# Kernel tuning notes

Measured on AMD Instinct MI355X. Metric: run time of the kernel, lower is better.

## Reference

```python
import jax, jax.numpy as jnp
import numpy as np

N, E = 50000, 800000
IN_CH, H, OUT_CH, ED, L = 64, 128, 128, 1, 4


def setup_inputs() -> dict:
    key = jax.random.key(0)
    ks = jax.random.split(key, 24)
    s = 0.02
    inp = {
        'h': jax.random.normal(ks[0], (N, IN_CH), jnp.float32),
        'coords': jax.random.normal(ks[1], (N, 3), jnp.float32),
        'edge_attr': jax.random.normal(ks[2], (E, ED), jnp.float32),
        'emb_in_W': jax.random.normal(ks[3], (IN_CH, H), jnp.float32) * s,
        'emb_in_b': jnp.zeros((H,), jnp.float32),
        'emb_out_W': jax.random.normal(ks[4], (H, OUT_CH), jnp.float32) * s,
        'emb_out_b': jnp.zeros((OUT_CH,), jnp.float32),
        # per-layer stacked params
        'eW1': jax.random.normal(ks[5], (L, 2 * H + 1 + ED, H), jnp.float32) * s,
        'eb1': jnp.zeros((L, H), jnp.float32),
        'eW2': jax.random.normal(ks[6], (L, H, H), jnp.float32) * s,
        'eb2': jnp.zeros((L, H), jnp.float32),
        'cW1': jax.random.normal(ks[7], (L, H, H), jnp.float32) * s,
        'cb1': jnp.zeros((L, H), jnp.float32),
        'cWc': jax.random.normal(ks[8], (L, H, 1), jnp.float32) * 0.001,  # xavier gain=0.001, no bias
        'nW1': jax.random.normal(ks[9], (L, 2 * H, H), jnp.float32) * s,
        'nb1': jnp.zeros((L, H), jnp.float32),
        'nW2': jax.random.normal(ks[10], (L, H, H), jnp.float32) * s,
        'nb2': jnp.zeros((L, H), jnp.float32),
        'edge_index': jax.random.randint(ks[11], (2, E), 0, N, jnp.int32),
    }
    return inp


def _egnn_forward(h, coords, edge_attr, emb_in_W, emb_in_b, emb_out_W, emb_out_b,
                  eW1, eb1, eW2, eb2, cW1, cb1, cWc, nW1, nb1, nW2, nb2, edge_index):
    silu = jax.nn.silu
    row, col = edge_index[0], edge_index[1]  # PyG: j=source=row, i=target=col
    # count of incoming edges per target node, for coords_agg='mean'
    counts = jax.ops.segment_sum(jnp.ones((E,), jnp.float32), col, num_segments=N)
    counts = jnp.maximum(counts, 1.0)[:, None]
    h = h @ emb_in_W + emb_in_b
    for l in range(L):
        coord_diff = coords[row] - coords[col]                       # [E,3]
        dist = jnp.sum(coord_diff * coord_diff, axis=-1, keepdims=True)  # [E,1]
        # message: edge MLP on cat(x_i, x_j, dist, edge_attr)
        edge_in = jnp.concatenate([h[col], h[row], dist, edge_attr], axis=-1)
        ef = silu(edge_in @ eW1[l] + eb1[l])
        ef = silu(ef @ eW2[l] + eb2[l])                               # [E,H]
        cw = silu(ef @ cW1[l] + cb1[l]) @ cWc[l]                      # [E,1]
        coord_upd = coord_diff * cw                                   # [E,3]
        # aggregate to target nodes
        agg_feat = jax.ops.segment_sum(ef, col, num_segments=N)       # [N,H]
        agg_coord = jax.ops.segment_sum(coord_upd, col, num_segments=N) / counts
        # node update (residual)
        node_in = jnp.concatenate([h, agg_feat], axis=-1)
        upd = silu(node_in @ nW1[l] + nb1[l]) @ nW2[l] + nb2[l]
        h = h + upd
        coords = coords + agg_coord
    h = h @ emb_out_W + emb_out_b
    return h, coords


def reference(h, coords, edge_attr, emb_in_W, emb_in_b, emb_out_W, emb_out_b,
              eW1, eb1, eW2, eb2, cW1, cb1, cWc, nW1, nb1, nW2, nb2, edge_index):
    return _egnn_forward(h, coords, edge_attr, emb_in_W, emb_in_b, emb_out_W, emb_out_b,
                         eW1, eb1, eW2, eb2, cW1, cb1, cWc, nW1, nb1, nW2, nb2, edge_index)
```

## Files before the change

kernel.cpp:

```cpp
#include <hip/hip_runtime.h>

constexpr int Nn = 50000;
constexpr int Ee = 800000;
constexpr int EIN_STR = 296;
constexpr int EF_STR  = 136;
constexpr int NIN_STR = 264;
constexpr int HIN_STR = 72;

typedef short s8v __attribute__((ext_vector_type(8)));
typedef float f4v __attribute__((ext_vector_type(4)));

__device__ __forceinline__ ushort f2bf(float f) {
    uint u = __float_as_uint(f);
    uint r = (u + 0x7FFFu + ((u >> 16) & 1u)) >> 16;
    return (ushort)r;
}
__device__ __forceinline__ float bf2f(ushort s) {
    return __uint_as_float(((uint)s) << 16);
}
__device__ __forceinline__ float silu_f(float x) {
    return x * __fdividef(1.0f, 1.0f + __expf(-x));
}

__global__ void __launch_bounds__(256) k_swzg(
    const float* __restrict__ src, ushort* __restrict__ dst, int K, int KC, int total)
{
    int gid = blockIdx.x * 256 + threadIdx.x;
    if (gid >= total) return;
    int per = KC * 4096;
    int l = gid / per, r = gid % per;
    int fb = r >> 9, rem = r & 511;
    int lane = rem >> 3, jj = rem & 7;
    int kc = fb >> 3, t = fb & 7;
    int k = kc * 32 + ((lane >> 4) << 3) + jj;
    int n = t * 16 + (lane & 15);
    float v = (k < K) ? src[(size_t)l * K * 128 + (size_t)k * 128 + n] : 0.0f;
    dst[gid] = f2bf(v);
}

__global__ void __launch_bounds__(256) k_count(const int* __restrict__ eidx, int* __restrict__ ecnt)
{
    int e = blockIdx.x * 256 + threadIdx.x;
    atomicAdd(&ecnt[eidx[Ee + e]], 1);
}

__global__ void __launch_bounds__(1024) k_scan(const int* __restrict__ ecnt, int* __restrict__ cursor)
{
    __shared__ int wsum[16];
    __shared__ int carry;
    int tid = threadIdx.x, lane = tid & 63, w = tid >> 6;
    if (tid == 0) carry = 0;
    __syncthreads();
    for (int start = 0; start < Nn; start += 1024) {
        int i = start + tid;
        int x = (i < Nn) ? ecnt[i] : 0;
        int c0 = carry;
        int s = x;
        #pragma unroll
        for (int off = 1; off < 64; off <<= 1) {
            int t = __shfl_up(s, off, 64);
            if (lane >= off) s += t;
        }
        if (lane == 63) wsum[w] = s;
        __syncthreads();
        if (w == 0) {
            int t = (lane < 16) ? wsum[lane] : 0;
            #pragma unroll
            for (int off = 1; off < 16; off <<= 1) {
                int u = __shfl_up(t, off, 64);
                if (lane >= off) t += u;
            }
            if (lane < 16) wsum[lane] = t;
        }
        __syncthreads();
        int woff = (w == 0) ? 0 : wsum[w - 1];
        if (i < Nn) cursor[i] = c0 + woff + s - x;
        int blocksum = wsum[15];
        __syncthreads();
        if (tid == 0) carry = c0 + blocksum;
        __syncthreads();
    }
}

__global__ void __launch_bounds__(256) k_scatter(
    const int* __restrict__ eidx, const float* __restrict__ edge_attr,
    int* __restrict__ cursor,
    int* __restrict__ srow, int* __restrict__ scol, float* __restrict__ sattr)
{
    int e = blockIdx.x * 256 + threadIdx.x;
    int r = eidx[e], c = eidx[Ee + e];
    int p = atomicAdd(&cursor[c], 1);
    srow[p] = r; scol[p] = c; sattr[p] = edge_attr[e];
}

__global__ void __launch_bounds__(512, 2) k_emb(
    const float* __restrict__ h_in, const float* __restrict__ coords,
    const ushort* __restrict__ ws_, const float* __restrict__ b,
    float* __restrict__ hbuf, ushort* __restrict__ hbf, float* __restrict__ cbuf)
{
    __shared__ alignas(16) ushort s_h[64 * HIN_STR];
    const int tid = threadIdx.x;
    const int nb = blockIdx.x * 64;
    #pragma unroll
    for (int i = 0; i < 2; i++) {
        int idx = i * 512 + tid;
        int e = idx >> 4, ch = idx & 15;
        int node = nb + e;
        float4 f = make_float4(0.f, 0.f, 0.f, 0.f);
        if (node < Nn) f = *(const float4*)(h_in + (size_t)node * 64 + ch * 4);
        ushort4 u; u.x = f2bf(f.x); u.y = f2bf(f.y); u.z = f2bf(f.z); u.w = f2bf(f.w);
        *(ushort4*)(s_h + e * HIN_STR + ch * 4) = u;
    }
    if (tid < 192) {
        int n = nb + tid / 3, d = tid % 3;
        if (n < Nn) cbuf[n * 3 + d] = coords[n * 3 + d];
    }
    __syncthreads();
    const int lane = tid & 63, wave = tid >> 6;
    const int m = lane & 15, quad = lane >> 4;
    const int ws2 = wave >> 2, wt = wave & 3;
    f4v acc[2][2];
    #pragma unroll
    for (int mt = 0; mt < 2; mt++) { acc[mt][0] = (f4v){0,0,0,0}; acc[mt][1] = (f4v){0,0,0,0}; }
    const ushort* bBase = ws_ + wt * 1024 + lane * 8;
    #pragma unroll
    for (int kc = 0; kc < 2; kc++) {
        s8v b0 = *(const s8v*)(bBase + kc * 4096);
        s8v b1v = *(const s8v*)(bBase + kc * 4096 + 512);
        #pragma unroll
        for (int mt = 0; mt < 2; mt++) {
            s8v a = *(const s8v*)(s_h + (ws2 * 32 + mt * 16 + m) * HIN_STR + kc * 32 + quad * 8);
            acc[mt][0] = __builtin_amdgcn_mfma_f32_16x16x32_bf16(a, b0, acc[mt][0], 0, 0, 0);
            acc[mt][1] = __builtin_amdgcn_mfma_f32_16x16x32_bf16(a, b1v, acc[mt][1], 0, 0, 0);
        }
    }
    #pragma unroll
    for (int tt = 0; tt < 2; tt++) {
        int col = (wt * 2 + tt) * 16 + m;
        float bias = b[col];
        #pragma unroll
        for (int mt = 0; mt < 2; mt++)
            #pragma unroll
            for (int r = 0; r < 4; r++) {
                int node = nb + ws2 * 32 + mt * 16 + quad * 4 + r;
                if (node < Nn) {
                    float v = acc[mt][tt][r] + bias;
                    hbuf[(size_t)node * 128 + col] = v;
                    hbf[(size_t)node * 128 + col] = f2bf(v);
                }
            }
    }
}

__global__ void __launch_bounds__(512, 2) k_edge(
    const ushort* __restrict__ hbf, const float* __restrict__ cbuf,
    const int* __restrict__ srow, const int* __restrict__ scol, const float* __restrict__ sattr,
    const ushort* __restrict__ w1s, const float* __restrict__ b1,
    const ushort* __restrict__ w2s, const float* __restrict__ b2,
    const ushort* __restrict__ cw1s, const float* __restrict__ cb1,
    const float* __restrict__ cwc,
    float* __restrict__ agg_feat, float* __restrict__ agg_coord)
{
    __shared__ alignas(16) ushort s_ein[64 * EIN_STR];
    __shared__ alignas(16) ushort s_efa[64 * EF_STR];
    __shared__ alignas(16) ushort s_efb[64 * EF_STR];
    __shared__ int   s_col[64];
    __shared__ int   s_row[64];
    __shared__ float s_cd[64 * 3];
    __shared__ float s_cw[64];

    const int tid = threadIdx.x;
    const int eb = blockIdx.x * 64;

    if (tid < 64) {
        int rw = srow[eb + tid], cl = scol[eb + tid];
        s_row[tid] = rw; s_col[tid] = cl;
        float d0 = cbuf[rw * 3 + 0] - cbuf[cl * 3 + 0];
        float d1 = cbuf[rw * 3 + 1] - cbuf[cl * 3 + 1];
        float d2 = cbuf[rw * 3 + 2] - cbuf[cl * 3 + 2];
        s_cd[tid * 3 + 0] = d0; s_cd[tid * 3 + 1] = d1; s_cd[tid * 3 + 2] = d2;
        float dist = d0 * d0 + d1 * d1 + d2 * d2;
        s_ein[tid * EIN_STR + 256] = f2bf(dist);
        s_ein[tid * EIN_STR + 257] = f2bf(sattr[eb + tid]);
        uint* zp = (uint*)(s_ein + tid * EIN_STR + 258);
        #pragma unroll
        for (int z = 0; z < 15; z++) zp[z] = 0;
        s_cw[tid] = 0.0f;
    }
    __syncthreads();

    #pragma unroll
    for (int i = 0; i < 4; i++) {
        int idx = i * 512 + tid;
        int e = idx >> 5, ch = idx & 31;
        int node = (ch < 16) ? s_col[e] : s_row[e];
        uint4 v = *(const uint4*)(hbf + (size_t)node * 128 + (ch & 15) * 8);
        *(uint4*)(s_ein + e * EIN_STR + ch * 8) = v;
    }
    __syncthreads();

    const int lane = tid & 63, wave = tid >> 6;
    const int m = lane & 15, quad = lane >> 4;
    const int ws2 = wave >> 2, wt = wave & 3;
    const int rbase = ws2 * 32;

    {
        f4v acc[2][2];
        #pragma unroll
        for (int mt = 0; mt < 2; mt++) { acc[mt][0] = (f4v){0,0,0,0}; acc[mt][1] = (f4v){0,0,0,0}; }
        const ushort* bBase = w1s + wt * 1024 + (size_t)lane * 8;
        #pragma unroll
        for (int kc = 0; kc < 9; kc++) {
            s8v b0 = *(const s8v*)(bBase + kc * 4096);
            s8v b1v = *(const s8v*)(bBase + kc * 4096 + 512);
            #pragma unroll
            for (int mt = 0; mt < 2; mt++) {
                s8v a = *(const s8v*)(s_ein + (rbase + mt * 16 + m) * EIN_STR + kc * 32 + quad * 8);
                acc[mt][0] = __builtin_amdgcn_mfma_f32_16x16x32_bf16(a, b0, acc[mt][0], 0, 0, 0);
                acc[mt][1] = __builtin_amdgcn_mfma_f32_16x16x32_bf16(a, b1v, acc[mt][1], 0, 0, 0);
            }
        }
        #pragma unroll
        for (int tt = 0; tt < 2; tt++) {
            int col = (wt * 2 + tt) * 16 + m;
            float bias = b1[col];
            #pragma unroll
            for (int mt = 0; mt < 2; mt++)
                #pragma unroll
                for (int r = 0; r < 4; r++)
                    s_efa[(rbase + mt * 16 + quad * 4 + r) * EF_STR + col] = f2bf(silu_f(acc[mt][tt][r] + bias));
        }
    }
    __syncthreads();

    {
        f4v acc[2][2];
        #pragma unroll
        for (int mt = 0; mt < 2; mt++) { acc[mt][0] = (f4v){0,0,0,0}; acc[mt][1] = (f4v){0,0,0,0}; }
        const ushort* bBase = w2s + wt * 1024 + (size_t)lane * 8;
        #pragma unroll
        for (int kc = 0; kc < 4; kc++) {
            s8v b0 = *(const s8v*)(bBase + kc * 4096);
            s8v b1v = *(const s8v*)(bBase + kc * 4096 + 512);
            #pragma unroll
            for (int mt = 0; mt < 2; mt++) {
                s8v a = *(const s8v*)(s_efa + (rbase + mt * 16 + m) * EF_STR + kc * 32 + quad * 8);
                acc[mt][0] = __builtin_amdgcn_mfma_f32_16x16x32_bf16(a, b0, acc[mt][0], 0, 0, 0);
                acc[mt][1] = __builtin_amdgcn_mfma_f32_16x16x32_bf16(a, b1v, acc[mt][1], 0, 0, 0);
            }
        }
        #pragma unroll
        for (int tt = 0; tt < 2; tt++) {
            int col = (wt * 2 + tt) * 16 + m;
            float bias = b2[col];
            #pragma unroll
            for (int mt = 0; mt < 2; mt++)
                #pragma unroll
                for (int r = 0; r < 4; r++)
                    s_efb[(rbase + mt * 16 + quad * 4 + r) * EF_STR + col] = f2bf(silu_f(acc[mt][tt][r] + bias));
        }
    }
    __syncthreads();

    {
        f4v acc[2][2];
        #pragma unroll
        for (int mt = 0; mt < 2; mt++) { acc[mt][0] = (f4v){0,0,0,0}; acc[mt][1] = (f4v){0,0,0,0}; }
        const ushort* bBase = cw1s + wt * 1024 + (size_t)lane * 8;
        #pragma unroll
        for (int kc = 0; kc < 4; kc++) {
            s8v b0 = *(const s8v*)(bBase + kc * 4096);
            s8v b1v = *(const s8v*)(bBase + kc * 4096 + 512);
            #pragma unroll
            for (int mt = 0; mt < 2; mt++) {
                s8v a = *(const s8v*)(s_efb + (rbase + mt * 16 + m) * EF_STR + kc * 32 + quad * 8);
                acc[mt][0] = __builtin_amdgcn_mfma_f32_16x16x32_bf16(a, b0, acc[mt][0], 0, 0, 0);
                acc[mt][1] = __builtin_amdgcn_mfma_f32_16x16x32_bf16(a, b1v, acc[mt][1], 0, 0, 0);
            }
        }
        int c0 = wt * 32 + m, c1 = wt * 32 + 16 + m;
        float bias0 = cb1[c0], wc0 = cwc[c0];
        float bias1 = cb1[c1], wc1 = cwc[c1];
        #pragma unroll
        for (int mt = 0; mt < 2; mt++) {
            float p0 = silu_f(acc[mt][0][0] + bias0) * wc0 + silu_f(acc[mt][1][0] + bias1) * wc1;
            float p1 = silu_f(acc[mt][0][1] + bias0) * wc0 + silu_f(acc[mt][1][1] + bias1) * wc1;
            float p2 = silu_f(acc[mt][0][2] + bias0) * wc0 + silu_f(acc[mt][1][2] + bias1) * wc1;
            float p3 = silu_f(acc[mt][0][3] + bias0) * wc0 + silu_f(acc[mt][1][3] + bias1) * wc1;
            #pragma unroll
            for (int off = 1; off < 16; off <<= 1) {
                p0 += __shfl_xor(p0, off, 64);
                p1 += __shfl_xor(p1, off, 64);
                p2 += __shfl_xor(p2, off, 64);
                p3 += __shfl_xor(p3, off, 64);
            }
            if (m < 4) {
                float v = (m == 0) ? p0 : (m == 1) ? p1 : (m == 2) ? p2 : p3;
                atomicAdd(&s_cw[rbase + mt * 16 + quad * 4 + m], v);
            }
        }
    }
    __syncthreads();

    if (tid < 12) {
        int d = tid % 3, seg = tid / 3;
        int e0 = seg * 16;
        float acc = 0.0f; int cur = s_col[e0];
        for (int e = e0; e < e0 + 16; e++) {
            int c = s_col[e];
            if (c != cur) {
                unsafeAtomicAdd(&agg_coord[cur * 3 + d], acc);
                acc = 0.0f; cur = c;
            }
            acc += s_cd[e * 3 + d] * s_cw[e];
        }
        unsafeAtomicAdd(&agg_coord[cur * 3 + d], acc);
    }

    {
        int j = tid & 127;
        int e0 = (tid >> 7) * 16;
        float acc = 0.0f; int cur = s_col[e0];
        #pragma unroll 4
        for (int e = e0; e < e0 + 16; e++) {
            int c = s_col[e];
            if (c != cur) {
                unsafeAtomicAdd(&agg_feat[(size_t)cur * 128 + j], acc);
                acc = 0.0f; cur = c;
            }
            acc += bf2f(s_efb[e * EF_STR + j]);
        }
        unsafeAtomicAdd(&agg_feat[(size_t)cur * 128 + j], acc);
    }
}

__global__ void __launch_bounds__(512, 2) k_node(
    float* __restrict__ hbuf, ushort* __restrict__ hbf, float* __restrict__ cbuf,
    const float* __restrict__ agg_feat, const float* __restrict__ agg_coord,
    const int* __restrict__ ecnt,
    const ushort* __restrict__ w1s, const float* __restrict__ b1,
    const ushort* __restrict__ w2s, const float* __restrict__ b2)
{
    __shared__ alignas(16) ushort s_nin[64 * NIN_STR];
    __shared__ alignas(16) ushort s_t1[64 * EF_STR];
    const int tid = threadIdx.x;
    const int nb = blockIdx.x * 64;

    #pragma unroll
    for (int i = 0; i < 2; i++) {
        int idx = i * 512 + tid;
        int e = idx >> 4, ch = idx & 15;
        int node = nb + e;
        uint4 v = make_uint4(0, 0, 0, 0);
        if (node < Nn) v = *(const uint4*)(hbf + (size_t)node * 128 + ch * 8);
        *(uint4*)(s_nin + e * NIN_STR + ch * 8) = v;
    }
    #pragma unroll
    for (int i = 0; i < 4; i++) {
        int idx = i * 512 + tid;
        int e = idx >> 5, ch = idx & 31;
        int node = nb + e;
        float4 f = make_float4(0.f, 0.f, 0.f, 0.f);
        if (node < Nn) f = *(const float4*)(agg_feat + (size_t)node * 128 + ch * 4);
        ushort4 u; u.x = f2bf(f.x); u.y = f2bf(f.y); u.z = f2bf(f.z); u.w = f2bf(f.w);
        *(ushort4*)(s_nin + e * NIN_STR + 128 + ch * 4) = u;
    }
    if (tid < 64) {
        int n = nb + tid;
        if (n < Nn) {
            float c = (float)ecnt[n]; c = (c < 1.0f) ? 1.0f : c;
            float inv = __fdividef(1.0f, c);
            cbuf[n * 3 + 0] += agg_coord[n * 3 + 0] * inv;
            cbuf[n * 3 + 1] += agg_coord[n * 3 + 1] * inv;
            cbuf[n * 3 + 2] += agg_coord[n * 3 + 2] * inv;
        }
    }
    __syncthreads();

    const int lane = tid & 63, wave = tid >> 6;
    const int m = lane & 15, quad = lane >> 4;
    const int ws2 = wave >> 2, wt = wave & 3;
    const int rbase = ws2 * 32;

    {
        f4v acc[2][2];
        #pragma unroll
        for (int mt = 0; mt < 2; mt++) { acc[mt][0] = (f4v){0,0,0,0}; acc[mt][1] = (f4v){0,0,0,0}; }
        const ushort* bBase = w1s + wt * 1024 + (size_t)lane * 8;
        #pragma unroll
        for (int kc = 0; kc < 8; kc++) {
            s8v b0 = *(const s8v*)(bBase + kc * 4096);
            s8v b1v = *(const s8v*)(bBase + kc * 4096 + 512);
            #pragma unroll
            for (int mt = 0; mt < 2; mt++) {
                s8v a = *(const s8v*)(s_nin + (rbase + mt * 16 + m) * NIN_STR + kc * 32 + quad * 8);
                acc[mt][0] = __builtin_amdgcn_mfma_f32_16x16x32_bf16(a, b0, acc[mt][0], 0, 0, 0);
                acc[mt][1] = __builtin_amdgcn_mfma_f32_16x16x32_bf16(a, b1v, acc[mt][1], 0, 0, 0);
            }
        }
        #pragma unroll
        for (int tt = 0; tt < 2; tt++) {
            int col = (wt * 2 + tt) * 16 + m;
            float bias = b1[col];
            #pragma unroll
            for (int mt = 0; mt < 2; mt++)
                #pragma unroll
                for (int r = 0; r < 4; r++)
                    s_t1[(rbase + mt * 16 + quad * 4 + r) * EF_STR + col] = f2bf(silu_f(acc[mt][tt][r] + bias));
        }
    }
    __syncthreads();

    {
        f4v acc[2][2];
        #pragma unroll
        for (int mt = 0; mt < 2; mt++) { acc[mt][0] = (f4v){0,0,0,0}; acc[mt][1] = (f4v){0,0,0,0}; }
        const ushort* bBase = w2s + wt * 1024 + (size_t)lane * 8;
        #pragma unroll
        for (int kc = 0; kc < 4; kc++) {
            s8v b0 = *(const s8v*)(bBase + kc * 4096);
            s8v b1v = *(const s8v*)(bBase + kc * 4096 + 512);
            #pragma unroll
            for (int mt = 0; mt < 2; mt++) {
                s8v a = *(const s8v*)(s_t1 + (rbase + mt * 16 + m) * EF_STR + kc * 32 + quad * 8);
                acc[mt][0] = __builtin_amdgcn_mfma_f32_16x16x32_bf16(a, b0, acc[mt][0], 0, 0, 0);
                acc[mt][1] = __builtin_amdgcn_mfma_f32_16x16x32_bf16(a, b1v, acc[mt][1], 0, 0, 0);
            }
        }
        #pragma unroll
        for (int tt = 0; tt < 2; tt++) {
            int col = (wt * 2 + tt) * 16 + m;
            float bias = b2[col];
            #pragma unroll
            for (int mt = 0; mt < 2; mt++)
                #pragma unroll
                for (int r = 0; r < 4; r++) {
                    int node = nb + rbase + mt * 16 + quad * 4 + r;
                    if (node < Nn) {
                        float v = hbuf[(size_t)node * 128 + col] + acc[mt][tt][r] + bias;
                        hbuf[(size_t)node * 128 + col] = v;
                        hbf[(size_t)node * 128 + col] = f2bf(v);
                    }
                }
        }
    }
}

__global__ void __launch_bounds__(512, 2) k_emb_out(
    const ushort* __restrict__ hbf, const float* __restrict__ cbuf,
    const ushort* __restrict__ ws_, const float* __restrict__ b, float* __restrict__ out)
{
    __shared__ alignas(16) ushort s_h[64 * EF_STR];
    const int tid = threadIdx.x;
    const int nb = blockIdx.x * 64;
    #pragma unroll
    for (int i = 0; i < 2; i++) {
        int idx = i * 512 + tid;
        int e = idx >> 4, ch = idx & 15;
        int node = nb + e;
        uint4 v = make_uint4(0, 0, 0, 0);
        if (node < Nn) v = *(const uint4*)(hbf + (size_t)node * 128 + ch * 8);
        *(uint4*)(s_h + e * EF_STR + ch * 8) = v;
    }
    if (tid < 192) {
        int n = nb + tid / 3, d = tid % 3;
        if (n < Nn) out[(size_t)Nn * 128 + n * 3 + d] = cbuf[n * 3 + d];
    }
    __syncthreads();
    const int lane = tid & 63, wave = tid >> 6;
    const int m = lane & 15, quad = lane >> 4;
    const int ws2 = wave >> 2, wt = wave & 3;
    f4v acc[2][2];
    #pragma unroll
    for (int mt = 0; mt < 2; mt++) { acc[mt][0] = (f4v){0,0,0,0}; acc[mt][1] = (f4v){0,0,0,0}; }
    const ushort* bBase = ws_ + wt * 1024 + (size_t)lane * 8;
    #pragma unroll
    for (int kc = 0; kc < 4; kc++) {
        s8v b0 = *(const s8v*)(bBase + kc * 4096);
        s8v b1v = *(const s8v*)(bBase + kc * 4096 + 512);
        #pragma unroll
        for (int mt = 0; mt < 2; mt++) {
            s8v a = *(const s8v*)(s_h + (ws2 * 32 + mt * 16 + m) * EF_STR + kc * 32 + quad * 8);
            acc[mt][0] = __builtin_amdgcn_mfma_f32_16x16x32_bf16(a, b0, acc[mt][0], 0, 0, 0);
            acc[mt][1] = __builtin_amdgcn_mfma_f32_16x16x32_bf16(a, b1v, acc[mt][1], 0, 0, 0);
        }
    }
    #pragma unroll
    for (int tt = 0; tt < 2; tt++) {
        int col = (wt * 2 + tt) * 16 + m;
        float bias = b[col];
        #pragma unroll
        for (int mt = 0; mt < 2; mt++)
            #pragma unroll
            for (int r = 0; r < 4; r++) {
                int node = nb + ws2 * 32 + mt * 16 + quad * 4 + r;
                if (node < Nn) out[(size_t)node * 128 + col] = acc[mt][tt][r] + bias;
            }
    }
}

extern "C" void kernel_launch(void* const* d_in, const int* in_sizes, int n_in,
                              void* d_out, int out_size, void* d_ws, size_t ws_size,
                              hipStream_t stream)
{
    const float* h_in      = (const float*)d_in[0];
    const float* coords    = (const float*)d_in[1];
    const float* edge_attr = (const float*)d_in[2];
    const float* emb_in_W  = (const float*)d_in[3];
    const float* emb_in_b  = (const float*)d_in[4];
    const float* emb_out_W = (const float*)d_in[5];
    const float* emb_out_b = (const float*)d_in[6];
    const float* eW1 = (const float*)d_in[7];
    const float* eb1 = (const float*)d_in[8];
    const float* eW2 = (const float*)d_in[9];
    const float* eb2 = (const float*)d_in[10];
    const float* cW1 = (const float*)d_in[11];
    const float* cb1 = (const float*)d_in[12];
    const float* cWc = (const float*)d_in[13];
    const float* nW1 = (const float*)d_in[14];
    const float* nb1 = (const float*)d_in[15];
    const float* nW2 = (const float*)d_in[16];
    const float* nb2 = (const float*)d_in[17];
    const int*  eidx = (const int*)d_in[18];

    size_t off = 0;
    char* base = (char*)d_ws;
    auto alloc = [&](size_t bytes) -> char* {
        char* p = base + off;
        off += (bytes + 255) & ~(size_t)255;
        return p;
    };
    float*  hbuf      = (float*)alloc((size_t)Nn * 128 * 4);
    ushort* hbf       = (ushort*)alloc((size_t)Nn * 128 * 2);
    float*  cbuf      = (float*)alloc((size_t)Nn * 3 * 4);
    int*    ecnt      = (int*)alloc((size_t)Nn * 4);
    int*    cursor    = (int*)alloc((size_t)Nn * 4);
    int*    srow      = (int*)alloc((size_t)Ee * 4);
    int*    scol      = (int*)alloc((size_t)Ee * 4);
    float*  sattr     = (float*)alloc((size_t)Ee * 4);
    float*  agg_feat  = (float*)alloc((size_t)Nn * 128 * 4);
    float*  agg_coord = (float*)alloc((size_t)Nn * 3 * 4);
    ushort* eW1s      = (ushort*)alloc((size_t)4 * 36864 * 2);
    ushort* eW2s      = (ushort*)alloc((size_t)4 * 16384 * 2);
    ushort* cW1s      = (ushort*)alloc((size_t)4 * 16384 * 2);
    ushort* nW1s      = (ushort*)alloc((size_t)4 * 32768 * 2);
    ushort* nW2s      = (ushort*)alloc((size_t)4 * 16384 * 2);
    ushort* eInWs     = (ushort*)alloc((size_t)8192 * 2);
    ushort* eOutWs    = (ushort*)alloc((size_t)16384 * 2);

    k_swzg<<<(4*9*4096+255)/256, 256, 0, stream>>>(eW1, eW1s, 258, 9, 4*9*4096);
    k_swzg<<<(4*4*4096+255)/256, 256, 0, stream>>>(eW2, eW2s, 128, 4, 4*4*4096);
    k_swzg<<<(4*4*4096+255)/256, 256, 0, stream>>>(cW1, cW1s, 128, 4, 4*4*4096);
    k_swzg<<<(4*8*4096+255)/256, 256, 0, stream>>>(nW1, nW1s, 256, 8, 4*8*4096);
    k_swzg<<<(4*4*4096+255)/256, 256, 0, stream>>>(nW2, nW2s, 128, 4, 4*4*4096);
    k_swzg<<<(2*4096+255)/256,   256, 0, stream>>>(emb_in_W,  eInWs,  64, 2, 2*4096);
    k_swzg<<<(4*4096+255)/256,   256, 0, stream>>>(emb_out_W, eOutWs, 128, 4, 4*4096);

    hipMemsetAsync(ecnt, 0, (size_t)Nn * 4, stream);
    k_count<<<Ee / 256, 256, 0, stream>>>(eidx, ecnt);
    k_scan<<<1, 1024, 0, stream>>>(ecnt, cursor);
    k_scatter<<<Ee / 256, 256, 0, stream>>>(eidx, edge_attr, cursor, srow, scol, sattr);
    k_emb<<<(Nn + 63) / 64, 512, 0, stream>>>(h_in, coords, eInWs, emb_in_b, hbuf, hbf, cbuf);

    for (int l = 0; l < 4; l++) {
        hipMemsetAsync(agg_feat, 0, (size_t)Nn * 128 * 4, stream);
        hipMemsetAsync(agg_coord, 0, (size_t)Nn * 3 * 4, stream);
        k_edge<<<Ee / 64, 512, 0, stream>>>(
            hbf, cbuf, srow, scol, sattr,
            eW1s + (size_t)l * 36864, eb1 + l * 128,
            eW2s + (size_t)l * 16384, eb2 + l * 128,
            cW1s + (size_t)l * 16384, cb1 + l * 128,
            cWc + l * 128,
            agg_feat, agg_coord);
        k_node<<<(Nn + 63) / 64, 512, 0, stream>>>(
            hbuf, hbf, cbuf, agg_feat, agg_coord, ecnt,
            nW1s + (size_t)l * 32768, nb1 + l * 128,
            nW2s + (size_t)l * 16384, nb2 + l * 128);
    }
    k_emb_out<<<(Nn + 63) / 64, 512, 0, stream>>>(hbf, cbuf, eOutWs, emb_out_b, (float*)d_out);
}
```

Baseline: 1.753 ms.

## Transpose MFMA operands, vectorize epilogues, shrink edge-kernel LDS, raise occupancy

Every GEMM now swaps the MFMA operands so weights act as A and activations as B. Each lane then holds four consecutive output columns of one row, which lets the epilogues use float4 bias loads, float4 stores and packed bf16 writes via perm. The edge kernel splits the concatenated input buffer into separate h_i/h_j tiles plus a small tail tile and reuses those buffers across stages, which cuts LDS use enough to raise launch bounds from 2 to 8 blocks. The coordinate weight reduction now writes per-wave partials to LDS instead of using shared atomics and a serial segment scan, so each edge issues its own global atomic. Intermediate activations use truncating bf16 conversion (pack2bf_t) instead of round-to-nearest-even, which changes precision slightly, and the higher occupancy risks register spills.

```diff
diff --git a/kernel.cpp b/kernel.cpp
--- a/kernel.cpp
+++ b/kernel.cpp
@@ -2,8 +2,8 @@
 
 constexpr int Nn = 50000;
 constexpr int Ee = 800000;
-constexpr int EIN_STR = 296;
 constexpr int EF_STR  = 136;
+constexpr int TL_STR  = 40;
 constexpr int NIN_STR = 264;
 constexpr int HIN_STR = 72;
 
@@ -20,6 +20,14 @@
 }
 __device__ __forceinline__ float silu_f(float x) {
     return x * __fdividef(1.0f, 1.0f + __expf(-x));
+}
+__device__ __forceinline__ uint pack2bf_t(float lo, float hi) {
+    return __builtin_amdgcn_perm(__float_as_uint(hi), __float_as_uint(lo), 0x07060302u);
+}
+__device__ __forceinline__ uint pack2bf_r(float lo, float hi) {
+    uint a = __float_as_uint(lo) + 0x8000u;
+    uint b = __float_as_uint(hi) + 0x8000u;
+    return __builtin_amdgcn_perm(b, a, 0x07060302u);
 }
 
 __global__ void __launch_bounds__(256) k_swzg(
@@ -119,40 +127,43 @@
     const int lane = tid & 63, wave = tid >> 6;
     const int m = lane & 15, quad = lane >> 4;
     const int ws2 = wave >> 2, wt = wave & 3;
+    const int rbase = ws2 * 32;
     f4v acc[2][2];
     #pragma unroll
-    for (int mt = 0; mt < 2; mt++) { acc[mt][0] = (f4v){0,0,0,0}; acc[mt][1] = (f4v){0,0,0,0}; }
-    const ushort* bBase = ws_ + wt * 1024 + lane * 8;
+    for (int nt = 0; nt < 2; nt++) { acc[nt][0] = (f4v){0,0,0,0}; acc[nt][1] = (f4v){0,0,0,0}; }
+    const ushort* aBase = ws_ + wt * 1024 + lane * 8;
     #pragma unroll
     for (int kc = 0; kc < 2; kc++) {
-        s8v b0 = *(const s8v*)(bBase + kc * 4096);
-        s8v b1v = *(const s8v*)(bBase + kc * 4096 + 512);
-        #pragma unroll
-        for (int mt = 0; mt < 2; mt++) {
-            s8v a = *(const s8v*)(s_h + (ws2 * 32 + mt * 16 + m) * HIN_STR + kc * 32 + quad * 8);
-            acc[mt][0] = __builtin_amdgcn_mfma_f32_16x16x32_bf16(a, b0, acc[mt][0], 0, 0, 0);
-            acc[mt][1] = __builtin_amdgcn_mfma_f32_16x16x32_bf16(a, b1v, acc[mt][1], 0, 0, 0);
-        }
-    }
-    #pragma unroll
-    for (int tt = 0; tt < 2; tt++) {
-        int col = (wt * 2 + tt) * 16 + m;
-        float bias = b[col];
-        #pragma unroll
-        for (int mt = 0; mt < 2; mt++)
-            #pragma unroll
-            for (int r = 0; r < 4; r++) {
-                int node = nb + ws2 * 32 + mt * 16 + quad * 4 + r;
-                if (node < Nn) {
-                    float v = acc[mt][tt][r] + bias;
-                    hbuf[(size_t)node * 128 + col] = v;
-                    hbf[(size_t)node * 128 + col] = f2bf(v);
-                }
-            }
-    }
-}
-
-__global__ void __launch_bounds__(512, 2) k_edge(
+        s8v a0 = *(const s8v*)(aBase + kc * 4096);
+        s8v a1 = *(const s8v*)(aBase + kc * 4096 + 512);
+        #pragma unroll
+        for (int nt = 0; nt < 2; nt++) {
+            s8v bf = *(const s8v*)(s_h + (rbase + nt * 16 + m) * HIN_STR + kc * 32 + quad * 8);
+            acc[nt][0] = __builtin_amdgcn_mfma_f32_16x16x32_bf16(a0, bf, acc[nt][0], 0, 0, 0);
+            acc[nt][1] = __builtin_amdgcn_mfma_f32_16x16x32_bf16(a1, bf, acc[nt][1], 0, 0, 0);
+        }
+    }
+    #pragma unroll
+    for (int nt = 0; nt < 2; nt++) {
+        int node = nb + rbase + nt * 16 + m;
+        if (node < Nn) {
+            #pragma unroll
+            for (int ct = 0; ct < 2; ct++) {
+                int colb = (wt * 2 + ct) * 16 + quad * 4;
+                float4 bb = *(const float4*)(b + colb);
+                float v0 = acc[nt][ct][0] + bb.x;
+                float v1 = acc[nt][ct][1] + bb.y;
+                float v2 = acc[nt][ct][2] + bb.z;
+                float v3 = acc[nt][ct][3] + bb.w;
+                *(float4*)(hbuf + (size_t)node * 128 + colb) = make_float4(v0, v1, v2, v3);
+                uint2 pk; pk.x = pack2bf_r(v0, v1); pk.y = pack2bf_r(v2, v3);
+                *(uint2*)(hbf + (size_t)node * 128 + colb) = pk;
+            }
+        }
+    }
+}
+
+__global__ void __launch_bounds__(512, 8) k_edge(
     const ushort* __restrict__ hbf, const float* __restrict__ cbuf,
     const int* __restrict__ srow, const int* __restrict__ scol, const float* __restrict__ sattr,
     const ushort* __restrict__ w1s, const float* __restrict__ b1,
@@ -161,41 +172,38 @@
     const float* __restrict__ cwc,
     float* __restrict__ agg_feat, float* __restrict__ agg_coord)
 {
-    __shared__ alignas(16) ushort s_ein[64 * EIN_STR];
-    __shared__ alignas(16) ushort s_efa[64 * EF_STR];
-    __shared__ alignas(16) ushort s_efb[64 * EF_STR];
+    __shared__ alignas(16) ushort s_a[64 * EF_STR];
+    __shared__ alignas(16) ushort s_b[64 * EF_STR];
+    __shared__ alignas(16) ushort s_t[64 * TL_STR];
     __shared__ int   s_col[64];
-    __shared__ int   s_row[64];
     __shared__ float s_cd[64 * 3];
-    __shared__ float s_cw[64];
 
     const int tid = threadIdx.x;
     const int eb = blockIdx.x * 64;
 
     if (tid < 64) {
         int rw = srow[eb + tid], cl = scol[eb + tid];
-        s_row[tid] = rw; s_col[tid] = cl;
+        s_col[tid] = cl;
         float d0 = cbuf[rw * 3 + 0] - cbuf[cl * 3 + 0];
         float d1 = cbuf[rw * 3 + 1] - cbuf[cl * 3 + 1];
         float d2 = cbuf[rw * 3 + 2] - cbuf[cl * 3 + 2];
         s_cd[tid * 3 + 0] = d0; s_cd[tid * 3 + 1] = d1; s_cd[tid * 3 + 2] = d2;
         float dist = d0 * d0 + d1 * d1 + d2 * d2;
-        s_ein[tid * EIN_STR + 256] = f2bf(dist);
-        s_ein[tid * EIN_STR + 257] = f2bf(sattr[eb + tid]);
-        uint* zp = (uint*)(s_ein + tid * EIN_STR + 258);
+        s_t[tid * TL_STR + 0] = f2bf(dist);
+        s_t[tid * TL_STR + 1] = f2bf(sattr[eb + tid]);
+        uint* zp = (uint*)(s_t + tid * TL_STR + 2);
         #pragma unroll
         for (int z = 0; z < 15; z++) zp[z] = 0;
-        s_cw[tid] = 0.0f;
-    }
-    __syncthreads();
-
+    }
     #pragma unroll
     for (int i = 0; i < 4; i++) {
         int idx = i * 512 + tid;
         int e = idx >> 5, ch = idx & 31;
-        int node = (ch < 16) ? s_col[e] : s_row[e];
+        int node = (ch < 16) ? scol[eb + e] : srow[eb + e];
         uint4 v = *(const uint4*)(hbf + (size_t)node * 128 + (ch & 15) * 8);
-        *(uint4*)(s_ein + e * EIN_STR + ch * 8) = v;
+        ushort* dst = (ch < 16) ? (s_a + e * EF_STR + ch * 8)
+                                : (s_b + e * EF_STR + (ch - 16) * 8);
+        *(uint4*)dst = v;
     }
     __syncthreads();
 
@@ -204,137 +212,160 @@
     const int ws2 = wave >> 2, wt = wave & 3;
     const int rbase = ws2 * 32;
 
+    f4v acc[2][2];
+    #pragma unroll
+    for (int nt = 0; nt < 2; nt++) { acc[nt][0] = (f4v){0,0,0,0}; acc[nt][1] = (f4v){0,0,0,0}; }
     {
-        f4v acc[2][2];
-        #pragma unroll
-        for (int mt = 0; mt < 2; mt++) { acc[mt][0] = (f4v){0,0,0,0}; acc[mt][1] = (f4v){0,0,0,0}; }
-        const ushort* bBase = w1s + wt * 1024 + (size_t)lane * 8;
-        #pragma unroll
-        for (int kc = 0; kc < 9; kc++) {
-            s8v b0 = *(const s8v*)(bBase + kc * 4096);
-            s8v b1v = *(const s8v*)(bBase + kc * 4096 + 512);
-            #pragma unroll
-            for (int mt = 0; mt < 2; mt++) {
-                s8v a = *(const s8v*)(s_ein + (rbase + mt * 16 + m) * EIN_STR + kc * 32 + quad * 8);
-                acc[mt][0] = __builtin_amdgcn_mfma_f32_16x16x32_bf16(a, b0, acc[mt][0], 0, 0, 0);
-                acc[mt][1] = __builtin_amdgcn_mfma_f32_16x16x32_bf16(a, b1v, acc[mt][1], 0, 0, 0);
-            }
-        }
-        #pragma unroll
-        for (int tt = 0; tt < 2; tt++) {
-            int col = (wt * 2 + tt) * 16 + m;
-            float bias = b1[col];
-            #pragma unroll
-            for (int mt = 0; mt < 2; mt++)
-                #pragma unroll
-                for (int r = 0; r < 4; r++)
-                    s_efa[(rbase + mt * 16 + quad * 4 + r) * EF_STR + col] = f2bf(silu_f(acc[mt][tt][r] + bias));
+        const ushort* aBase = w1s + wt * 1024 + (size_t)lane * 8;
+        #pragma unroll
+        for (int kc = 0; kc < 4; kc++) {
+            s8v a0 = *(const s8v*)(aBase + kc * 4096);
+            s8v a1 = *(const s8v*)(aBase + kc * 4096 + 512);
+            #pragma unroll
+            for (int nt = 0; nt < 2; nt++) {
+                s8v bf = *(const s8v*)(s_a + (rbase + nt * 16 + m) * EF_STR + kc * 32 + quad * 8);
+                acc[nt][0] = __builtin_amdgcn_mfma_f32_16x16x32_bf16(a0, bf, acc[nt][0], 0, 0, 0);
+                acc[nt][1] = __builtin_amdgcn_mfma_f32_16x16x32_bf16(a1, bf, acc[nt][1], 0, 0, 0);
+            }
+        }
+        #pragma unroll
+        for (int kc = 4; kc < 8; kc++) {
+            s8v a0 = *(const s8v*)(aBase + kc * 4096);
+            s8v a1 = *(const s8v*)(aBase + kc * 4096 + 512);
+            #pragma unroll
+            for (int nt = 0; nt < 2; nt++) {
+                s8v bf = *(const s8v*)(s_b + (rbase + nt * 16 + m) * EF_STR + (kc - 4) * 32 + quad * 8);
+                acc[nt][0] = __builtin_amdgcn_mfma_f32_16x16x32_bf16(a0, bf, acc[nt][0], 0, 0, 0);
+                acc[nt][1] = __builtin_amdgcn_mfma_f32_16x16x32_bf16(a1, bf, acc[nt][1], 0, 0, 0);
+            }
+        }
+        {
+            s8v a0 = *(const s8v*)(aBase + 8 * 4096);
+            s8v a1 = *(const s8v*)(aBase + 8 * 4096 + 512);
+            #pragma unroll
+            for (int nt = 0; nt < 2; nt++) {
+                s8v bf = *(const s8v*)(s_t + (rbase + nt * 16 + m) * TL_STR + quad * 8);
+                acc[nt][0] = __builtin_amdgcn_mfma_f32_16x16x32_bf16(a0, bf, acc[nt][0], 0, 0, 0);
+                acc[nt][1] = __builtin_amdgcn_mfma_f32_16x16x32_bf16(a1, bf, acc[nt][1], 0, 0, 0);
+            }
+        }
+    }
+    __syncthreads();
+
+    #pragma unroll
+    for (int nt = 0; nt < 2; nt++) {
+        int edge = rbase + nt * 16 + m;
+        #pragma unroll
+        for (int ct = 0; ct < 2; ct++) {
+            int colb = (wt * 2 + ct) * 16 + quad * 4;
+            float4 bb = *(const float4*)(b1 + colb);
+            float v0 = silu_f(acc[nt][ct][0] + bb.x);
+            float v1 = silu_f(acc[nt][ct][1] + bb.y);
+            float v2 = silu_f(acc[nt][ct][2] + bb.z);
+            float v3 = silu_f(acc[nt][ct][3] + bb.w);
+            uint2 pk; pk.x = pack2bf_t(v0, v1); pk.y = pack2bf_t(v2, v3);
+            *(uint2*)(s_a + edge * EF_STR + colb) = pk;
         }
     }
     __syncthreads();
 
     {
-        f4v acc[2][2];
-        #pragma unroll
-        for (int mt = 0; mt < 2; mt++) { acc[mt][0] = (f4v){0,0,0,0}; acc[mt][1] = (f4v){0,0,0,0}; }
-        const ushort* bBase = w2s + wt * 1024 + (size_t)lane * 8;
+        f4v acc2[2][2];
+        #pragma unroll
+        for (int nt = 0; nt < 2; nt++) { acc2[nt][0] = (f4v){0,0,0,0}; acc2[nt][1] = (f4v){0,0,0,0}; }
+        const ushort* aBase = w2s + wt * 1024 + (size_t)lane * 8;
         #pragma unroll
         for (int kc = 0; kc < 4; kc++) {
-            s8v b0 = *(const s8v*)(bBase + kc * 4096);
-            s8v b1v = *(const s8v*)(bBase + kc * 4096 + 512);
-            #pragma unroll
-            for (int mt = 0; mt < 2; mt++) {
-                s8v a = *(const s8v*)(s_efa + (rbase + mt * 16 + m) * EF_STR + kc * 32 + quad * 8);
-                acc[mt][0] = __builtin_amdgcn_mfma_f32_16x16x32_bf16(a, b0, acc[mt][0], 0, 0, 0);
-                acc[mt][1] = __builtin_amdgcn_mfma_f32_16x16x32_bf16(a, b1v, acc[mt][1], 0, 0, 0);
-            }
-        }
-        #pragma unroll
-        for (int tt = 0; tt < 2; tt++) {
-            int col = (wt * 2 + tt) * 16 + m;
-            float bias = b2[col];
-            #pragma unroll
-            for (int mt = 0; mt < 2; mt++)
-                #pragma unroll
-                for (int r = 0; r < 4; r++)
-                    s_efb[(rbase + mt * 16 + quad * 4 + r) * EF_STR + col] = f2bf(silu_f(acc[mt][tt][r] + bias));
+            s8v a0 = *(const s8v*)(aBase + kc * 4096);
+            s8v a1 = *(const s8v*)(aBase + kc * 4096 + 512);
+            #pragma unroll
+            for (int nt = 0; nt < 2; nt++) {
+                s8v bf = *(const s8v*)(s_a + (rbase + nt * 16 + m) * EF_STR + kc * 32 + quad * 8);
+                acc2[nt][0] = __builtin_amdgcn_mfma_f32_16x16x32_bf16(a0, bf, acc2[nt][0], 0, 0, 0);
+                acc2[nt][1] = __builtin_amdgcn_mfma_f32_16x16x32_bf16(a1, bf, acc2[nt][1], 0, 0, 0);
+            }
+        }
+        #pragma unroll
+        for (int nt = 0; nt < 2; nt++) {
+            int edge = rbase + nt * 16 + m;
+            #pragma unroll
+            for (int ct = 0; ct < 2; ct++) {
+                int colb = (wt * 2 + ct) * 16 + quad * 4;
+                float4 bb = *(const float4*)(b2 + colb);
+                float v0 = silu_f(acc2[nt][ct][0] + bb.x);
+                float v1 = silu_f(acc2[nt][ct][1] + bb.y);
+                float v2 = silu_f(acc2[nt][ct][2] + bb.z);
+                float v3 = silu_f(acc2[nt][ct][3] + bb.w);
+                uint2 pk; pk.x = pack2bf_t(v0, v1); pk.y = pack2bf_t(v2, v3);
+                *(uint2*)(s_b + edge * EF_STR + colb) = pk;
+            }
         }
     }
     __syncthreads();
 
     {
-        f4v acc[2][2];
-        #pragma unroll
-        for (int mt = 0; mt < 2; mt++) { acc[mt][0] = (f4v){0,0,0,0}; acc[mt][1] = (f4v){0,0,0,0}; }
-        const ushort* bBase = cw1s + wt * 1024 + (size_t)lane * 8;
+        f4v acc3[2][2];
+        #pragma unroll
+        for (int nt = 0; nt < 2; nt++) { acc3[nt][0] = (f4v){0,0,0,0}; acc3[nt][1] = (f4v){0,0,0,0}; }
+        const ushort* aBase = cw1s + wt * 1024 + (size_t)lane * 8;
         #pragma unroll
         for (int kc = 0; kc < 4; kc++) {
-            s8v b0 = *(const s8v*)(bBase + kc * 4096);
-            s8v b1v = *(const s8v*)(bBase + kc * 4096 + 512);
-            #pragma unroll
-            for (int mt = 0; mt < 2; mt++) {
-                s8v a = *(const s8v*)(s_efb + (rbase + mt * 16 + m) * EF_STR + kc * 32 + quad * 8);
-                acc[mt][0] = __builtin_amdgcn_mfma_f32_16x16x32_bf16(a, b0, acc[mt][0], 0, 0, 0);
-                acc[mt][1] = __builtin_amdgcn_mfma_f32_16x16x32_bf16(a, b1v, acc[mt][1], 0, 0, 0);
-            }
-        }
-        int c0 = wt * 32 + m, c1 = wt * 32 + 16 + m;
-        float bias0 = cb1[c0], wc0 = cwc[c0];
-        float bias1 = cb1[c1], wc1 = cwc[c1];
-        #pragma unroll
-        for (int mt = 0; mt < 2; mt++) {
-            float p0 = silu_f(acc[mt][0][0] + bias0) * wc0 + silu_f(acc[mt][1][0] + bias1) * wc1;
-            float p1 = silu_f(acc[mt][0][1] + bias0) * wc0 + silu_f(acc[mt][1][1] + bias1) * wc1;
-            float p2 = silu_f(acc[mt][0][2] + bias0) * wc0 + silu_f(acc[mt][1][2] + bias1) * wc1;
-            float p3 = silu_f(acc[mt][0][3] + bias0) * wc0 + silu_f(acc[mt][1][3] + bias1) * wc1;
-            #pragma unroll
-            for (int off = 1; off < 16; off <<= 1) {
-                p0 += __shfl_xor(p0, off, 64);
-                p1 += __shfl_xor(p1, off, 64);
-                p2 += __shfl_xor(p2, off, 64);
-                p3 += __shfl_xor(p3, off, 64);
-            }
-            if (m < 4) {
-                float v = (m == 0) ? p0 : (m == 1) ? p1 : (m == 2) ? p2 : p3;
-                atomicAdd(&s_cw[rbase + mt * 16 + quad * 4 + m], v);
-            }
-        }
-    }
-    __syncthreads();
-
-    if (tid < 12) {
-        int d = tid % 3, seg = tid / 3;
-        int e0 = seg * 16;
-        float acc = 0.0f; int cur = s_col[e0];
-        for (int e = e0; e < e0 + 16; e++) {
-            int c = s_col[e];
-            if (c != cur) {
-                unsafeAtomicAdd(&agg_coord[cur * 3 + d], acc);
-                acc = 0.0f; cur = c;
-            }
-            acc += s_cd[e * 3 + d] * s_cw[e];
-        }
-        unsafeAtomicAdd(&agg_coord[cur * 3 + d], acc);
-    }
-
+            s8v a0 = *(const s8v*)(aBase + kc * 4096);
+            s8v a1 = *(const s8v*)(aBase + kc * 4096 + 512);
+            #pragma unroll
+            for (int nt = 0; nt < 2; nt++) {
+                s8v bf = *(const s8v*)(s_b + (rbase + nt * 16 + m) * EF_STR + kc * 32 + quad * 8);
+                acc3[nt][0] = __builtin_amdgcn_mfma_f32_16x16x32_bf16(a0, bf, acc3[nt][0], 0, 0, 0);
+                acc3[nt][1] = __builtin_amdgcn_mfma_f32_16x16x32_bf16(a1, bf, acc3[nt][1], 0, 0, 0);
+            }
+        }
+        float* s_part = (float*)s_t;
+        #pragma unroll
+        for (int nt = 0; nt < 2; nt++) {
+            float p = 0.0f;
+            #pragma unroll
+            for (int ct = 0; ct < 2; ct++) {
+                int colb = (wt * 2 + ct) * 16 + quad * 4;
+                float4 cb = *(const float4*)(cb1 + colb);
+                float4 wc = *(const float4*)(cwc + colb);
+                p += silu_f(acc3[nt][ct][0] + cb.x) * wc.x;
+                p += silu_f(acc3[nt][ct][1] + cb.y) * wc.y;
+                p += silu_f(acc3[nt][ct][2] + cb.z) * wc.z;
+                p += silu_f(acc3[nt][ct][3] + cb.w) * wc.w;
+            }
+            p += __shfl_xor(p, 16, 64);
+            p += __shfl_xor(p, 32, 64);
+            if (quad == 0) s_part[(rbase + nt * 16 + m) * 20 + wt] = p;
+        }
+    }
+    __syncthreads();
+
+    if (tid < 64) {
+        float4 sp = *(const float4*)((const float*)s_t + tid * 20);
+        float cw = sp.x + sp.y + sp.z + sp.w;
+        int cn = s_col[tid];
+        unsafeAtomicAdd(&agg_coord[cn * 3 + 0], s_cd[tid * 3 + 0] * cw);
+        unsafeAtomicAdd(&agg_coord[cn * 3 + 1], s_cd[tid * 3 + 1] * cw);
+        unsafeAtomicAdd(&agg_coord[cn * 3 + 2], s_cd[tid * 3 + 2] * cw);
+    }
     {
         int j = tid & 127;
         int e0 = (tid >> 7) * 16;
-        float acc = 0.0f; int cur = s_col[e0];
+        float accv = 0.0f; int cur = s_col[e0];
         #pragma unroll 4
         for (int e = e0; e < e0 + 16; e++) {
             int c = s_col[e];
             if (c != cur) {
-                unsafeAtomicAdd(&agg_feat[(size_t)cur * 128 + j], acc);
-                acc = 0.0f; cur = c;
-            }
-            acc += bf2f(s_efb[e * EF_STR + j]);
-        }
-        unsafeAtomicAdd(&agg_feat[(size_t)cur * 128 + j], acc);
-    }
-}
-
-__global__ void __launch_bounds__(512, 2) k_node(
+                unsafeAtomicAdd(&agg_feat[(size_t)cur * 128 + j], accv);
+                accv = 0.0f; cur = c;
+            }
+            accv += bf2f(s_b[e * EF_STR + j]);
+        }
+        unsafeAtomicAdd(&agg_feat[(size_t)cur * 128 + j], accv);
+    }
+}
+
+__global__ void __launch_bounds__(512, 6) k_node(
     float* __restrict__ hbuf, ushort* __restrict__ hbf, float* __restrict__ cbuf,
     const float* __restrict__ agg_feat, const float* __restrict__ agg_coord,
     const int* __restrict__ ecnt,
@@ -362,8 +393,8 @@
         int node = nb + e;
         float4 f = make_float4(0.f, 0.f, 0.f, 0.f);
         if (node < Nn) f = *(const float4*)(agg_feat + (size_t)node * 128 + ch * 4);
-        ushort4 u; u.x = f2bf(f.x); u.y = f2bf(f.y); u.z = f2bf(f.z); u.w = f2bf(f.w);
-        *(ushort4*)(s_nin + e * NIN_STR + 128 + ch * 4) = u;
+        uint2 pk; pk.x = pack2bf_t(f.x, f.y); pk.y = pack2bf_t(f.z, f.w);
+        *(uint2*)(s_nin + e * NIN_STR + 128 + ch * 4) = pk;
     }
     if (tid < 64) {
         int n = nb + tid;
@@ -385,28 +416,33 @@
     {
         f4v acc[2][2];
         #pragma unroll
-        for (int mt = 0; mt < 2; mt++) { acc[mt][0] = (f4v){0,0,0,0}; acc[mt][1] = (f4v){0,0,0,0}; }
-        const ushort* bBase = w1s + wt * 1024 + (size_t)lane * 8;
+        for (int nt = 0; nt < 2; nt++) { acc[nt][0] = (f4v){0,0,0,0}; acc[nt][1] = (f4v){0,0,0,0}; }
+        const ushort* aBase = w1s + wt * 1024 + (size_t)lane * 8;
         #pragma unroll
         for (int kc = 0; kc < 8; kc++) {
-            s8v b0 = *(const s8v*)(bBase + kc * 4096);
-            s8v b1v = *(const s8v*)(bBase + kc * 4096 + 512);
-            #pragma unroll
-            for (int mt = 0; mt < 2; mt++) {
-                s8v a = *(const s8v*)(s_nin + (rbase + mt * 16 + m) * NIN_STR + kc * 32 + quad * 8);
-                acc[mt][0] = __builtin_amdgcn_mfma_f32_16x16x32_bf16(a, b0, acc[mt][0], 0, 0, 0);
-                acc[mt][1] = __builtin_amdgcn_mfma_f32_16x16x32_bf16(a, b1v, acc[mt][1], 0, 0, 0);
-            }
-        }
-        #pragma unroll
-        for (int tt = 0; tt < 2; tt++) {
-            int col = (wt * 2 + tt) * 16 + m;
-            float bias = b1[col];
-            #pragma unroll
-            for (int mt = 0; mt < 2; mt++)
-                #pragma unroll
-                for (int r = 0; r < 4; r++)
-                    s_t1[(rbase + mt * 16 + quad * 4 + r) * EF_STR + col] = f2bf(silu_f(acc[mt][tt][r] + bias));
+            s8v a0 = *(const s8v*)(aBase + kc * 4096);
+            s8v a1 = *(const s8v*)(aBase + kc * 4096 + 512);
+            #pragma unroll
+            for (int nt = 0; nt < 2; nt++) {
+                s8v bf = *(const s8v*)(s_nin + (rbase + nt * 16 + m) * NIN_STR + kc * 32 + quad * 8);
+                acc[nt][0] = __builtin_amdgcn_mfma_f32_16x16x32_bf16(a0, bf, acc[nt][0], 0, 0, 0);
+                acc[nt][1] = __builtin_amdgcn_mfma_f32_16x16x32_bf16(a1, bf, acc[nt][1], 0, 0, 0);
+            }
+        }
+        #pragma unroll
+        for (int nt = 0; nt < 2; nt++) {
+            int row = rbase + nt * 16 + m;
+            #pragma unroll
+            for (int ct = 0; ct < 2; ct++) {
+                int colb = (wt * 2 + ct) * 16 + quad * 4;
+                float4 bb = *(const float4*)(b1 + colb);
+                float v0 = silu_f(acc[nt][ct][0] + bb.x);
+                float v1 = silu_f(acc[nt][ct][1] + bb.y);
+                float v2 = silu_f(acc[nt][ct][2] + bb.z);
+                float v3 = silu_f(acc[nt][ct][3] + bb.w);
+                uint2 pk; pk.x = pack2bf_t(v0, v1); pk.y = pack2bf_t(v2, v3);
+                *(uint2*)(s_t1 + row * EF_STR + colb) = pk;
+            }
         }
     }
     __syncthreads();
@@ -414,34 +450,37 @@
     {
         f4v acc[2][2];
         #pragma unroll
-        for (int mt = 0; mt < 2; mt++) { acc[mt][0] = (f4v){0,0,0,0}; acc[mt][1] = (f4v){0,0,0,0}; }
-        const ushort* bBase = w2s + wt * 1024 + (size_t)lane * 8;
+        for (int nt = 0; nt < 2; nt++) { acc[nt][0] = (f4v){0,0,0,0}; acc[nt][1] = (f4v){0,0,0,0}; }
+        const ushort* aBase = w2s + wt * 1024 + (size_t)lane * 8;
         #pragma unroll
         for (int kc = 0; kc < 4; kc++) {
-            s8v b0 = *(const s8v*)(bBase + kc * 4096);
-            s8v b1v = *(const s8v*)(bBase + kc * 4096 + 512);
-            #pragma unroll
-            for (int mt = 0; mt < 2; mt++) {
-                s8v a = *(const s8v*)(s_t1 + (rbase + mt * 16 + m) * EF_STR + kc * 32 + quad * 8);
-                acc[mt][0] = __builtin_amdgcn_mfma_f32_16x16x32_bf16(a, b0, acc[mt][0], 0, 0, 0);
-                acc[mt][1] = __builtin_amdgcn_mfma_f32_16x16x32_bf16(a, b1v, acc[mt][1], 0, 0, 0);
-            }
-        }
-        #pragma unroll
-        for (int tt = 0; tt < 2; tt++) {
-            int col = (wt * 2 + tt) * 16 + m;
-            float bias = b2[col];
-            #pragma unroll
-            for (int mt = 0; mt < 2; mt++)
+            s8v a0 = *(const s8v*)(aBase + kc * 4096);
+            s8v a1 = *(const s8v*)(aBase + kc * 4096 + 512);
+            #pragma unroll
+            for (int nt = 0; nt < 2; nt++) {
+                s8v bf = *(const s8v*)(s_t1 + (rbase + nt * 16 + m) * EF_STR + kc * 32 + quad * 8);
+                acc[nt][0] = __builtin_amdgcn_mfma_f32_16x16x32_bf16(a0, bf, acc[nt][0], 0, 0, 0);
+                acc[nt][1] = __builtin_amdgcn_mfma_f32_16x16x32_bf16(a1, bf, acc[nt][1], 0, 0, 0);
+            }
+        }
+        #pragma unroll
+        for (int nt = 0; nt < 2; nt++) {
+            int node = nb + rbase + nt * 16 + m;
+            if (node < Nn) {
                 #pragma unroll
-                for (int r = 0; r < 4; r++) {
-                    int node = nb + rbase + mt * 16 + quad * 4 + r;
-                    if (node < Nn) {
-                        float v = hbuf[(size_t)node * 128 + col] + acc[mt][tt][r] + bias;
-                        hbuf[(size_t)node * 128 + col] = v;
-                        hbf[(size_t)node * 128 + col] = f2bf(v);
-                    }
+                for (int ct = 0; ct < 2; ct++) {
+                    int colb = (wt * 2 + ct) * 16 + quad * 4;
+                    float4 bb = *(const float4*)(b2 + colb);
+                    float4 old = *(const float4*)(hbuf + (size_t)node * 128 + colb);
+                    float v0 = old.x + acc[nt][ct][0] + bb.x;
+                    float v1 = old.y + acc[nt][ct][1] + bb.y;
+                    float v2 = old.z + acc[nt][ct][2] + bb.z;
+                    float v3 = old.w + acc[nt][ct][3] + bb.w;
+                    *(float4*)(hbuf + (size_t)node * 128 + colb) = make_float4(v0, v1, v2, v3);
+                    uint2 pk; pk.x = pack2bf_r(v0, v1); pk.y = pack2bf_r(v2, v3);
+                    *(uint2*)(hbf + (size_t)node * 128 + colb) = pk;
                 }
+            }
         }
     }
 }
@@ -470,32 +509,35 @@
     const int lane = tid & 63, wave = tid >> 6;
     const int m = lane & 15, quad = lane >> 4;
     const int ws2 = wave >> 2, wt = wave & 3;
+    const int rbase = ws2 * 32;
     f4v acc[2][2];
     #pragma unroll
-    for (int mt = 0; mt < 2; mt++) { acc[mt][0] = (f4v){0,0,0,0}; acc[mt][1] = (f4v){0,0,0,0}; }
-    const ushort* bBase = ws_ + wt * 1024 + (size_t)lane * 8;
+    for (int nt = 0; nt < 2; nt++) { acc[nt][0] = (f4v){0,0,0,0}; acc[nt][1] = (f4v){0,0,0,0}; }
+    const ushort* aBase = ws_ + wt * 1024 + (size_t)lane * 8;
     #pragma unroll
     for (int kc = 0; kc < 4; kc++) {
-        s8v b0 = *(const s8v*)(bBase + kc * 4096);
-        s8v b1v = *(const s8v*)(bBase + kc * 4096 + 512);
-        #pragma unroll
-        for (int mt = 0; mt < 2; mt++) {
-            s8v a = *(const s8v*)(s_h + (ws2 * 32 + mt * 16 + m) * EF_STR + kc * 32 + quad * 8);
-            acc[mt][0] = __builtin_amdgcn_mfma_f32_16x16x32_bf16(a, b0, acc[mt][0], 0, 0, 0);
-            acc[mt][1] = __builtin_amdgcn_mfma_f32_16x16x32_bf16(a, b1v, acc[mt][1], 0, 0, 0);
-        }
-    }
-    #pragma unroll
-    for (int tt = 0; tt < 2; tt++) {
-        int col = (wt * 2 + tt) * 16 + m;
-        float bias = b[col];
-        #pragma unroll
-        for (int mt = 0; mt < 2; mt++)
-            #pragma unroll
-            for (int r = 0; r < 4; r++) {
-                int node = nb + ws2 * 32 + mt * 16 + quad * 4 + r;
-                if (node < Nn) out[(size_t)node * 128 + col] = acc[mt][tt][r] + bias;
-            }
+        s8v a0 = *(const s8v*)(aBase + kc * 4096);
+        s8v a1 = *(const s8v*)(aBase + kc * 4096 + 512);
+        #pragma unroll
+        for (int nt = 0; nt < 2; nt++) {
+            s8v bf = *(const s8v*)(s_h + (rbase + nt * 16 + m) * EF_STR + kc * 32 + quad * 8);
+            acc[nt][0] = __builtin_amdgcn_mfma_f32_16x16x32_bf16(a0, bf, acc[nt][0], 0, 0, 0);
+            acc[nt][1] = __builtin_amdgcn_mfma_f32_16x16x32_bf16(a1, bf, acc[nt][1], 0, 0, 0);
+        }
+    }
+    #pragma unroll
+    for (int nt = 0; nt < 2; nt++) {
+        int node = nb + rbase + nt * 16 + m;
+        if (node < Nn) {
+            #pragma unroll
+            for (int ct = 0; ct < 2; ct++) {
+                int colb = (wt * 2 + ct) * 16 + quad * 4;
+                float4 bb = *(const float4*)(b + colb);
+                float4 o = make_float4(acc[nt][ct][0] + bb.x, acc[nt][ct][1] + bb.y,
+                                       acc[nt][ct][2] + bb.z, acc[nt][ct][3] + bb.w);
+                *(float4*)(out + (size_t)node * 128 + colb) = o;
+            }
+        }
     }
 }
 
```

Result: slower. 1.837 ms (+4.8%).
